# Performance work log

Hardware: AMD Instinct MI355X
Metric: run time of the kernel (lower is better)

The kernel has to match this reference:

```python
import jax, jax.numpy as jnp
import numpy as np

N = 262144       # nodes (4096 graphs * graph_deg 64)
E = 4194304      # edges
D = 64           # node_dim
DEPTH = 3
GRAPH_DEG = 64


def gcn_conv(x, W, b, src, dst, w):
    """PyG GCNConv with self-loops + symmetric norm; masked edges have w=0."""
    h = x @ W                                             # [N, D]
    deg = jax.ops.segment_sum(w, dst, num_segments=N) + 1.0  # +1 self-loop
    dinv = jax.lax.rsqrt(deg)                             # deg >= 1
    norm = dinv[src] * w * dinv[dst]                      # [E]
    agg = jax.ops.segment_sum(h[src] * norm[:, None], dst, num_segments=N)
    agg = agg + h * (dinv * dinv)[:, None]                # self-loop term
    return agg + b


def setup_inputs() -> dict:
    key = jax.random.key(0)
    ks = jax.random.split(key, 24)

    def xavier(k, fan_in, fan_out):
        lim = np.sqrt(6.0 / (fan_in + fan_out))
        return jax.random.uniform(k, (fan_in, fan_out), jnp.float32, -lim, lim)

    inp = {
        "x": jax.random.normal(ks[0], (N, 1), jnp.float32),
        "edge_index": jax.random.randint(ks[1], (2, E), 0, N, jnp.int64),
        "edge_types": jax.random.randint(ks[2], (E,), 0, 5, jnp.int64),
        "node_W": xavier(ks[3], 1, D), "node_b": jnp.zeros((D,), jnp.float32),
        "out1_W": xavier(ks[4], D, D), "out1_b": jnp.zeros((D,), jnp.float32),
        "out2_W": xavier(ks[5], D, 1), "out2_b": jnp.zeros((1,), jnp.float32),
    }
    names = ["W1", "W2", "W3", "W4", "W2b", "W3b", "W4b"]
    for i, n in enumerate(names):
        inp[n] = xavier(ks[6 + i], D, D)
        inp["b" + n[1:]] = jnp.zeros((D,), jnp.float32)
    return inp


def reference(x, edge_index, edge_types,
              node_W, node_b,
              W1, b1, W2, b2, W3, b3, W4, b4,
              W2b, b2b, W3b, b3b, W4b, b4b,
              out1_W, out1_b, out2_W, out2_b):
    src, dst = edge_index[0], edge_index[1]
    w1 = (edge_types == 1).astype(jnp.float32)
    w2 = (edge_types == 2).astype(jnp.float32)
    w3 = (edge_types == 3).astype(jnp.float32)
    w4 = (edge_types == 4).astype(jnp.float32)

    h = x @ node_W + node_b                               # [N, D]
    for _ in range(DEPTH):
        h_new = (gcn_conv(h, W1, b1, src, dst, w1)
                 + gcn_conv(h, W2, b2, src, dst, w2)
                 + gcn_conv(h, W3, b3, src, dst, w3)
                 + gcn_conv(h, W4, b4, src, dst, w4)
                 + gcn_conv(h, W2b, b2b, dst, src, w2)    # reversed edges
                 + gcn_conv(h, W3b, b3b, dst, src, w3)
                 + gcn_conv(h, W4b, b4b, dst, src, w4))
        h = jax.nn.relu(h_new)

    g = h.reshape(-1, GRAPH_DEG, D)                       # [B, deg, D]
    g = jnp.max(g, axis=1)                                # [B, D]
    g = jax.nn.relu(g @ out1_W + out1_b)
    return g @ out2_W + out2_b                            # [B, 1]
```

## Files before the change

kernel.cpp:

```cpp
#include <hip/hip_runtime.h>
#include <stdint.h>

typedef unsigned int u32;
typedef unsigned short u16;
typedef __attribute__((ext_vector_type(8))) short bf16x8;
typedef __attribute__((ext_vector_type(4))) float f32x4;

#define BCAP 16384u

struct Ptr7 { const float* p[7]; };

__device__ __forceinline__ int rfl(int v) { return __builtin_amdgcn_readfirstlane(v); }
__device__ __forceinline__ u16 f2bf(float f) {
    u32 u = __float_as_uint(f);
    u32 r = (u + 0x7FFFu + ((u >> 16) & 1u)) >> 16;
    return (u16)r;
}
__device__ __forceinline__ float bf2f(u16 h) { return __uint_as_float((u32)h << 16); }


__global__ void k_init_cur(u32* __restrict__ g) {
    int i = blockIdx.x * 256 + threadIdx.x;
    if (i < 512) g[i] = (u32)i << 14;
}

__global__ __launch_bounds__(256)
void k_passA(const int* __restrict__ ei, const int* __restrict__ ty, int E,
             u32* __restrict__ gcursor, u32* __restrict__ tmpItems) {
    __shared__ u32 hist[512], gb[512], cur[512];
    int tid = threadIdx.x;
    int e0 = blockIdx.x * 4096;
    int s[16], d[16], t[16];
#pragma unroll
    for (int i = 0; i < 16; i++) {
        int e = e0 + i * 256 + tid;
        if (e < E) { s[i] = ei[e]; d[i] = ei[E + e]; t[i] = ty[e]; }
        else t[i] = 0;
    }
    hist[tid] = 0; hist[tid + 256] = 0;
    __syncthreads();
#pragma unroll
    for (int i = 0; i < 16; i++) {
        if (t[i] >= 1) atomicAdd(&hist[(u32)d[i] >> 9], 1u);
        if (t[i] >= 2) atomicAdd(&hist[(u32)s[i] >> 9], 1u);
    }
    __syncthreads();
    u32 h0 = hist[tid], h1 = hist[tid + 256];
    gb[tid] = h0 ? atomicAdd(&gcursor[tid], h0) : 0u;
    gb[tid + 256] = h1 ? atomicAdd(&gcursor[tid + 256], h1) : 0u;
    cur[tid] = 0; cur[tid + 256] = 0;
    __syncthreads();
#pragma unroll
    for (int i = 0; i < 16; i++) {
        if (t[i] >= 1) {
            u32 b = (u32)d[i] >> 9;
            u32 slot = atomicAdd(&cur[b], 1u);
            u32 pos = gb[b] + slot;
            if (pos < ((b + 1u) << 14))
                tmpItems[pos] = (u32)s[i] | ((u32)(t[i] - 1) << 18) | (((u32)d[i] & 511u) << 21);
        }
        if (t[i] >= 2) {
            u32 b = (u32)s[i] >> 9;
            u32 slot = atomicAdd(&cur[b], 1u);
            u32 pos = gb[b] + slot;
            if (pos < ((b + 1u) << 14))
                tmpItems[pos] = (u32)d[i] | ((u32)(t[i] + 2) << 18) | (((u32)s[i] & 511u) << 21);
        }
    }
}

__global__ __launch_bounds__(256)
void k_passB(const u32* __restrict__ tmpItems, const u32* __restrict__ bucketEnd,
             float* __restrict__ dinv, u16* __restrict__ dinv16,
             u32* __restrict__ kcnt, int N) {
    __shared__ u32 c[512 * 8];
    int b = blockIdx.x, tid = threadIdx.x;
    for (int i = tid; i < 4096; i += 256) c[i] = 0;
    __syncthreads();
    u32 beg = (u32)b << 14;
    u32 end = bucketEnd[b];
    u32 cap = beg + BCAP;
    if (end > cap) end = cap;
    for (u32 i = beg + tid; i < end; i += 256) {
        u32 it = tmpItems[i];
        atomicAdd(&c[(it >> 21) * 8 + ((it >> 18) & 7)], 1u);
    }
    __syncthreads();
    int nodeBase = b << 9;
    for (int i = tid; i < 4096; i += 256) kcnt[(size_t)b * 4096 + i] = c[i];
    for (int l = tid; l < 512; l += 256) {
        int n = nodeBase + l;
#pragma unroll
        for (int k = 0; k < 7; k++) {
            float v = rsqrtf(1.0f + (float)c[l * 8 + k]);
            dinv[k * N + n] = v;
            dinv16[k * N + n] = f2bf(v);
        }
    }
}

__global__ __launch_bounds__(256)
void k_scan1(const u32* __restrict__ kcnt, u32* __restrict__ kofs, u32* __restrict__ bsums) {
    __shared__ u32 lds[256];
    int t = threadIdx.x;
    size_t base = (size_t)blockIdx.x * 8192 + (size_t)t * 32;
    u32 v[32];
    u32 s = 0;
    const uint4* src = (const uint4*)(kcnt + base);
#pragma unroll
    for (int q = 0; q < 8; q++) {
        uint4 c4 = src[q];
        v[q * 4 + 0] = s; s += c4.x;
        v[q * 4 + 1] = s; s += c4.y;
        v[q * 4 + 2] = s; s += c4.z;
        v[q * 4 + 3] = s; s += c4.w;
    }
    lds[t] = s; __syncthreads();
    for (int off = 1; off < 256; off <<= 1) {
        u32 x2 = (t >= off) ? lds[t - off] : 0u;
        __syncthreads();
        lds[t] += x2;
        __syncthreads();
    }
    u32 texcl = lds[t] - s;
    uint4* dst = (uint4*)(kofs + base);
#pragma unroll
    for (int q = 0; q < 8; q++) {
        uint4 o;
        o.x = v[q * 4 + 0] + texcl; o.y = v[q * 4 + 1] + texcl;
        o.z = v[q * 4 + 2] + texcl; o.w = v[q * 4 + 3] + texcl;
        dst[q] = o;
    }
    if (t == 255) bsums[blockIdx.x] = lds[255];
}

__global__ void k_scan2(const u32* __restrict__ bsums, u32* __restrict__ bexcl, int nb) {
    __shared__ u32 lds[256];
    int t = threadIdx.x;
    u32 v = (t < nb) ? bsums[t] : 0u;
    lds[t] = v; __syncthreads();
    for (int off = 1; off < 256; off <<= 1) {
        u32 x2 = (t >= off) ? lds[t - off] : 0u;
        __syncthreads();
        lds[t] += x2;
        __syncthreads();
    }
    if (t < nb) bexcl[t] = lds[t] - v;
}

__global__ __launch_bounds__(256)
void k_scan3(u32* __restrict__ kofs, const u32* __restrict__ bexcl,
             const u32* __restrict__ bsums, u32 M) {
    int t = threadIdx.x;
    size_t base = (size_t)blockIdx.x * 8192 + (size_t)t * 32;
    u32 add = bexcl[blockIdx.x];
    uint4* p4 = (uint4*)(kofs + base);
#pragma unroll
    for (int q = 0; q < 8; q++) {
        uint4 o = p4[q];
        o.x += add; o.y += add; o.z += add; o.w += add;
        p4[q] = o;
    }
    if (blockIdx.x == 255 && t == 255) kofs[M] = add + bsums[255];
}

__global__ __launch_bounds__(256)
void k_passC(const u32* __restrict__ tmpItems, const u32* __restrict__ bucketEnd,
             const u32* __restrict__ kofs, u32* __restrict__ entries) {
    __shared__ u32 cur[4096];
    int b = blockIdx.x, tid = threadIdx.x;
    for (int i = tid; i < 4096; i += 256) cur[i] = kofs[(size_t)b * 4096 + i];
    __syncthreads();
    u32 beg = (u32)b << 14;
    u32 end = bucketEnd[b];
    u32 cap = beg + BCAP;
    if (end > cap) end = cap;
    for (u32 i = beg + tid; i < end; i += 256) {
        u32 it = tmpItems[i];
        u32 k = (it >> 18) & 7u;
        u32 src = it & 0x3FFFFu;
        u32 p = atomicAdd(&cur[(it >> 21) * 8 + k], 1u);
        entries[p] = (k << 28) | (src << 7);
    }
}

__global__ __launch_bounds__(256)
void k_coef_pq(const u32* __restrict__ entries, const u32* __restrict__ kofs,
               const u16* __restrict__ dinv16, const float* __restrict__ dinv,
               const float* __restrict__ x, u16* __restrict__ coef16,
               float* __restrict__ P, float* __restrict__ Q, int N) {
    int i = blockIdx.x * 256 + threadIdx.x;
    u32 beg = kofs[i], end = kofs[i + 1];
    int k = i & 7, n = i >> 3;
    float sP = 0.f, sQ = 0.f;
    for (u32 p = beg; p < end; ++p) {
        u32 src = (entries[p] >> 7) & 0x3FFFFu;
        u16 cb = dinv16[(size_t)k * N + src];
        coef16[p] = cb;
        float cf = bf2f(cb);
        sP += cf * x[src];
        sQ += cf;
    }
    if (k < 7) {
        float dk = dinv[k * N + n];
        float xn = x[n];
        P[i] = dk * (sP + dk * xn);
        Q[i] = dk * (sQ + dk);
    }
}

__global__ void k_bsum(Ptr7 b, float* __restrict__ bsum) {
    int d = threadIdx.x;
    float s = 0.f;
#pragma unroll
    for (int k = 0; k < 7; k++) s += b.p[k][d];
    bsum[d] = s;
}

__global__ void k_uv(const float* __restrict__ nW, const float* __restrict__ nb,
                     Ptr7 W, float* __restrict__ U, float* __restrict__ V) {
    int k = blockIdx.x, d = threadIdx.x;
    const float* Wk = W.p[k];
    float u = 0.f, v = 0.f;
#pragma unroll 8
    for (int j = 0; j < 64; j++) {
        float w = Wk[j * 64 + d];
        u += nW[j] * w;
        v += nb[j] * w;
    }
    U[k * 64 + d] = u;
    V[k * 64 + d] = v;
}

__global__ void k_packW(Ptr7 W, u16* __restrict__ Wp) {
    int k = blockIdx.x;
    int tid = threadIdx.x;
    int ks = tid >> 8, ct = (tid >> 6) & 3, l = tid & 63;
    const float* Wk = W.p[k];
    u16* dst = Wp + (((size_t)(k * 2 + ks) * 4 + ct) * 512 + l * 8);
    int row0 = ks * 32 + (l >> 4) * 8;
    int col = ct * 16 + (l & 15);
#pragma unroll
    for (int i = 0; i < 8; i++) dst[i] = f2bf(Wk[(row0 + i) * 64 + col]);
}

__global__ __launch_bounds__(256)
void k_h1(const float* __restrict__ P, const float* __restrict__ Q,
          const float* __restrict__ U, const float* __restrict__ V,
          const float* __restrict__ bsum, u16* __restrict__ h1) {
    int i = blockIdx.x * 256 + threadIdx.x;
    int n = rfl(i >> 6);
    int d = i & 63;
    float acc = bsum[d];
#pragma unroll
    for (int k = 0; k < 7; k++)
        acc += P[n * 8 + k] * U[k * 64 + d] + Q[n * 8 + k] * V[k * 64 + d];
    h1[((size_t)n << 6) + d] = f2bf(fmaxf(acc, 0.f));
}

#define GACC(PK, CB, HV)                                             \
    {                                                                \
        float cf_ = __uint_as_float((u32)(CB) << 16);                \
        switch ((PK) >> 28) {                                        \
            case 0: a0 = fmaf(cf_, (HV), a0); break;                 \
            case 1: a1 = fmaf(cf_, (HV), a1); break;                 \
            case 2: a2 = fmaf(cf_, (HV), a2); break;                 \
            case 3: a3 = fmaf(cf_, (HV), a3); break;                 \
            case 4: a4 = fmaf(cf_, (HV), a4); break;                 \
            case 5: a5 = fmaf(cf_, (HV), a5); break;                 \
            default: a6 = fmaf(cf_, (HV), a6); break;                \
        }                                                            \
    }
#define HLOAD(PK) bf2f(*(const u16*)(hb + ((PK) & 0x01FFFFFFu)))

__global__ __launch_bounds__(256)
void k_gather(const u16* __restrict__ h, const u32* __restrict__ entries,
              const u16* __restrict__ coef16, const u32* __restrict__ kofs,
              const float* __restrict__ dinv, u16* __restrict__ m, int N, int c0) {
    int lane = threadIdx.x & 63;
    int nl = blockIdx.x * 4 + (threadIdx.x >> 6);
    int n = c0 + nl;
    const char* hb = (const char*)h + 2 * lane;
    u32 beg = (u32)rfl((int)kofs[(size_t)n << 3]);
    u32 end = (u32)rfl((int)kofs[((size_t)n << 3) + 7]);
    float hv = bf2f(h[((size_t)n << 6) + lane]);
    float d0 = dinv[n],         d1 = dinv[N + n],     d2 = dinv[2 * N + n];
    float d3 = dinv[3 * N + n], d4 = dinv[4 * N + n], d5 = dinv[5 * N + n];
    float d6 = dinv[6 * N + n];
    float a0 = d0 * hv, a1 = d1 * hv, a2 = d2 * hv, a3 = d3 * hv;
    float a4 = d4 * hv, a5 = d5 * hv, a6 = d6 * hv;

    u32 base = beg;
    u32 e = 0, cfw = 0;
    if (base + (u32)lane < end) {
        e = __builtin_nontemporal_load(&entries[base + lane]);
        cfw = (u32)__builtin_nontemporal_load(&coef16[base + lane]);
    }
    while (base < end) {
        u32 rem = end - base;
        int cnt = (rem < 64u) ? (int)rem : 64;
        u32 nb2 = base + 64;
        u32 en = 0, cfn = 0;
        if (nb2 + (u32)lane < end) {
            en = __builtin_nontemporal_load(&entries[nb2 + lane]);
            cfn = (u32)__builtin_nontemporal_load(&coef16[nb2 + lane]);
        }
        int j = 0;
        for (; j + 8 <= cnt; j += 8) {
            u32 pk0 = (u32)__builtin_amdgcn_readlane((int)e, j + 0);
            u32 pk1 = (u32)__builtin_amdgcn_readlane((int)e, j + 1);
            u32 pk2 = (u32)__builtin_amdgcn_readlane((int)e, j + 2);
            u32 pk3 = (u32)__builtin_amdgcn_readlane((int)e, j + 3);
            u32 pk4 = (u32)__builtin_amdgcn_readlane((int)e, j + 4);
            u32 pk5 = (u32)__builtin_amdgcn_readlane((int)e, j + 5);
            u32 pk6 = (u32)__builtin_amdgcn_readlane((int)e, j + 6);
            u32 pk7 = (u32)__builtin_amdgcn_readlane((int)e, j + 7);
            u32 cb0 = (u32)__builtin_amdgcn_readlane((int)cfw, j + 0);
            u32 cb1 = (u32)__builtin_amdgcn_readlane((int)cfw, j + 1);
            u32 cb2 = (u32)__builtin_amdgcn_readlane((int)cfw, j + 2);
            u32 cb3 = (u32)__builtin_amdgcn_readlane((int)cfw, j + 3);
            u32 cb4 = (u32)__builtin_amdgcn_readlane((int)cfw, j + 4);
            u32 cb5 = (u32)__builtin_amdgcn_readlane((int)cfw, j + 5);
            u32 cb6 = (u32)__builtin_amdgcn_readlane((int)cfw, j + 6);
            u32 cb7 = (u32)__builtin_amdgcn_readlane((int)cfw, j + 7);
            float h0 = HLOAD(pk0);
            float h1v = HLOAD(pk1);
            float h2v = HLOAD(pk2);
            float h3v = HLOAD(pk3);
            float h4v = HLOAD(pk4);
            float h5v = HLOAD(pk5);
            float h6v = HLOAD(pk6);
            float h7v = HLOAD(pk7);
            GACC(pk0, cb0, h0)
            GACC(pk1, cb1, h1v)
            GACC(pk2, cb2, h2v)
            GACC(pk3, cb3, h3v)
            GACC(pk4, cb4, h4v)
            GACC(pk5, cb5, h5v)
            GACC(pk6, cb6, h6v)
            GACC(pk7, cb7, h7v)
        }
        for (; j + 4 <= cnt; j += 4) {
            u32 pk0 = (u32)__builtin_amdgcn_readlane((int)e, j + 0);
            u32 pk1 = (u32)__builtin_amdgcn_readlane((int)e, j + 1);
            u32 pk2 = (u32)__builtin_amdgcn_readlane((int)e, j + 2);
            u32 pk3 = (u32)__builtin_amdgcn_readlane((int)e, j + 3);
            u32 cb0 = (u32)__builtin_amdgcn_readlane((int)cfw, j + 0);
            u32 cb1 = (u32)__builtin_amdgcn_readlane((int)cfw, j + 1);
            u32 cb2 = (u32)__builtin_amdgcn_readlane((int)cfw, j + 2);
            u32 cb3 = (u32)__builtin_amdgcn_readlane((int)cfw, j + 3);
            float h0 = HLOAD(pk0);
            float h1v = HLOAD(pk1);
            float h2v = HLOAD(pk2);
            float h3v = HLOAD(pk3);
            GACC(pk0, cb0, h0)
            GACC(pk1, cb1, h1v)
            GACC(pk2, cb2, h2v)
            GACC(pk3, cb3, h3v)
        }
        for (; j < cnt; ++j) {
            u32 pk = (u32)__builtin_amdgcn_readlane((int)e, j);
            u32 cb = (u32)__builtin_amdgcn_readlane((int)cfw, j);
            float hval = HLOAD(pk);
            GACC(pk, cb, hval)
        }
        e = en; cfw = cfn; base = nb2;
    }

    u16* mp = m + (size_t)nl * 448 + lane;
    __builtin_nontemporal_store(f2bf(d0 * a0), mp);
    __builtin_nontemporal_store(f2bf(d1 * a1), mp + 64);
    __builtin_nontemporal_store(f2bf(d2 * a2), mp + 128);
    __builtin_nontemporal_store(f2bf(d3 * a3), mp + 192);
    __builtin_nontemporal_store(f2bf(d4 * a4), mp + 256);
    __builtin_nontemporal_store(f2bf(d5 * a5), mp + 320);
    __builtin_nontemporal_store(f2bf(d6 * a6), mp + 384);
}

__global__ __launch_bounds__(256)
void k_gemm(const u16* __restrict__ m, const u16* __restrict__ Wp,
            const float* __restrict__ bsum, u16* __restrict__ hout, int c0) {
    int tid = threadIdx.x;
    int w = tid >> 6, l = tid & 63;
    int nb = blockIdx.x << 6;
    const u16* arow = m + (size_t)(nb + (w << 4) + (l & 15)) * 448 + ((l >> 4) << 3);
    const u16* bp = Wp + (size_t)l * 8;
    f32x4 acc0 = {0,0,0,0}, acc1 = {0,0,0,0}, acc2 = {0,0,0,0}, acc3 = {0,0,0,0};
#pragma unroll
    for (int kk = 0; kk < 14; kk++) {
        bf16x8 a  = __builtin_nontemporal_load((const bf16x8*)(arow + kk * 32));
        bf16x8 b0 = *(const bf16x8*)(bp + (size_t)(kk * 4 + 0) * 512);
        bf16x8 b1 = *(const bf16x8*)(bp + (size_t)(kk * 4 + 1) * 512);
        bf16x8 b2 = *(const bf16x8*)(bp + (size_t)(kk * 4 + 2) * 512);
        bf16x8 b3 = *(const bf16x8*)(bp + (size_t)(kk * 4 + 3) * 512);
        acc0 = __builtin_amdgcn_mfma_f32_16x16x32_bf16(a, b0, acc0, 0, 0, 0);
        acc1 = __builtin_amdgcn_mfma_f32_16x16x32_bf16(a, b1, acc1, 0, 0, 0);
        acc2 = __builtin_amdgcn_mfma_f32_16x16x32_bf16(a, b2, acc2, 0, 0, 0);
        acc3 = __builtin_amdgcn_mfma_f32_16x16x32_bf16(a, b3, acc3, 0, 0, 0);
    }
    int rl = (l >> 4) << 2, cl = l & 15;
    int rowg = c0 + nb + (w << 4) + rl;
    f32x4 accs[4] = {acc0, acc1, acc2, acc3};
#pragma unroll
    for (int ct = 0; ct < 4; ct++) {
        int col = ct * 16 + cl;
        float bv = bsum[col];
#pragma unroll
        for (int reg = 0; reg < 4; reg++) {
            float vv = fmaxf(accs[ct][reg] + bv, 0.f);
            hout[(size_t)(rowg + reg) * 64 + col] = f2bf(vv);
        }
    }
}

__global__ __launch_bounds__(256)
void k_head(const u16* __restrict__ h, const float* __restrict__ w1,
            const float* __restrict__ b1, const float* __restrict__ w2,
            const float* __restrict__ b2, float* __restrict__ out) {
    __shared__ float gmax[4][64];
    __shared__ float gl[64];
    __shared__ float t1p[4][64];
    int b = blockIdx.x;
    int tid = threadIdx.x;
    int d = tid & 63, rg = tid >> 6;
    const u16* hb = h + (size_t)b * 64 * 64;
    float pm = -1e30f;
#pragma unroll
    for (int i = 0; i < 16; i++) pm = fmaxf(pm, bf2f(hb[(rg * 16 + i) * 64 + d]));
    gmax[rg][d] = pm; __syncthreads();
    if (rg == 0) gl[d] = fmaxf(fmaxf(gmax[0][d], gmax[1][d]), fmaxf(gmax[2][d], gmax[3][d]));
    __syncthreads();
    float s = 0.f;
#pragma unroll
    for (int i = 0; i < 16; i++) { int dd = rg * 16 + i; s += gl[dd] * w1[dd * 64 + d]; }
    t1p[rg][d] = s; __syncthreads();
    if (rg == 0) {
        float t1 = fmaxf(t1p[0][d] + t1p[1][d] + t1p[2][d] + t1p[3][d] + b1[d], 0.f);
        float v = t1 * w2[d];
        for (int off = 32; off; off >>= 1) v += __shfl_down(v, off, 64);
        if (d == 0) out[b] = v + b2[0];
    }
}

extern "C" void kernel_launch(void* const* d_in, const int* in_sizes, int n_in,
                              void* d_out, int out_size, void* d_ws, size_t ws_size,
                              hipStream_t stream) {
    const float* x     = (const float*)d_in[0];
    const int*   ei    = (const int*)d_in[1];
    const int*   ty    = (const int*)d_in[2];
    const float* nodeW = (const float*)d_in[3];
    const float* nodeb = (const float*)d_in[4];
    const float* out1W = (const float*)d_in[5];
    const float* out1b = (const float*)d_in[6];
    const float* out2W = (const float*)d_in[7];
    const float* out2b = (const float*)d_in[8];

    Ptr7 W, B;
    W.p[0] = (const float*)d_in[9];  B.p[0] = (const float*)d_in[10];
    W.p[1] = (const float*)d_in[11]; B.p[1] = (const float*)d_in[12];
    W.p[2] = (const float*)d_in[13]; B.p[2] = (const float*)d_in[14];
    W.p[3] = (const float*)d_in[15]; B.p[3] = (const float*)d_in[16];
    W.p[4] = (const float*)d_in[17]; B.p[4] = (const float*)d_in[18];
    W.p[5] = (const float*)d_in[19]; B.p[5] = (const float*)d_in[20];
    W.p[6] = (const float*)d_in[21]; B.p[6] = (const float*)d_in[22];

    const int N = in_sizes[0];
    const int E = in_sizes[2];

    char* p = (char*)d_ws;
    auto carve = [&](size_t bytes) { void* r = (void*)p; p += (bytes + 255) & ~(size_t)255; return r; };
    u16*   hA       = (u16*)carve((size_t)N * 64 * 2);
    u16*   hB       = (u16*)carve((size_t)N * 64 * 2);
    u32*   entries  = (u32*)carve((size_t)2 * E * 4 + 256);
    u16*   coef16   = (u16*)carve((size_t)2 * E * 2 + 128);
    float* dinv     = (float*)carve((size_t)7 * N * 4);
    u16*   dinv16   = (u16*)carve((size_t)7 * N * 2);
    u32*   kcnt     = (u32*)carve((size_t)8 * N * 4);
    u32*   kofs     = (u32*)carve(((size_t)8 * N + 1) * 4);
    float* P        = (float*)carve((size_t)N * 8 * 4);
    float* Q        = (float*)carve((size_t)N * 8 * 4);
    float* U        = (float*)carve(7 * 64 * 4);
    float* V        = (float*)carve(7 * 64 * 4);
    float* bsum     = (float*)carve(256);
    u16*   Wp       = (u16*)carve((size_t)7 * 2 * 4 * 512 * 2);
    u32*   gcursor  = (u32*)carve(512 * 4);
    u32*   bsums    = (u32*)carve(1024);
    u32*   bexcl    = (u32*)carve(1024);
    size_t used = (size_t)(p - (char*)d_ws);
    size_t avail = (ws_size > used) ? (ws_size - used) : 0;
    u32*   tmpItems = (u32*)p;
    u16*   m        = (u16*)p;
    size_t chunkNodes = (avail / (448 * 2)) & ~(size_t)63;
    if (chunkNodes < 64) chunkNodes = 64;
    if (chunkNodes > 131072) chunkNodes = 131072;
    if (chunkNodes > (size_t)N) chunkNodes = (size_t)N;
    (void)n_in; (void)out_size;

    k_init_cur<<<2, 256, 0, stream>>>(gcursor);
    k_passA<<<(E + 4095) / 4096, 256, 0, stream>>>(ei, ty, E, gcursor, tmpItems);
    k_passB<<<512, 256, 0, stream>>>(tmpItems, gcursor, dinv, dinv16, kcnt, N);
    k_scan1<<<256, 256, 0, stream>>>(kcnt, kofs, bsums);
    k_scan2<<<1, 256, 0, stream>>>(bsums, bexcl, 256);
    k_scan3<<<256, 256, 0, stream>>>(kofs, bexcl, bsums, (u32)8 * N);
    k_passC<<<512, 256, 0, stream>>>(tmpItems, gcursor, kofs, entries);
    k_coef_pq<<<(8 * N) / 256, 256, 0, stream>>>(entries, kofs, dinv16, dinv, x,
                                                 coef16, P, Q, N);

    k_bsum<<<1, 64, 0, stream>>>(B, bsum);
    k_uv<<<7, 64, 0, stream>>>(nodeW, nodeb, W, U, V);
    k_packW<<<7, 512, 0, stream>>>(W, Wp);

    k_h1<<<(N * 64) / 256, 256, 0, stream>>>(P, Q, U, V, bsum, hA);

    u16* hcur = hA;
    u16* hnext = hB;
    for (int depth = 0; depth < 2; depth++) {
        for (int c0 = 0; c0 < N; c0 += (int)chunkNodes) {
            int cn = (int)(((size_t)(N - c0) < chunkNodes) ? (size_t)(N - c0) : chunkNodes);
            k_gather<<<cn / 4, 256, 0, stream>>>(hcur, entries, coef16, kofs, dinv, m, N, c0);
            k_gemm<<<cn / 64, 256, 0, stream>>>(m, Wp, bsum, hnext, c0);
        }
        u16* t = hcur; hcur = hnext; hnext = t;
    }

    k_head<<<N / 64, 256, 0, stream>>>(hcur, out1W, out1b, out2W, out2b, (float*)d_out);
}
```

Measured before the change: 943.5 us.

## Pad per-node edge lists to multiples of eight and use scalar loads in gather

The degree pass now writes a padding count into the eighth key slot so each node's edge segment is padded to a multiple of eight entries, and coef/PQ skips that slot. The gather kernel replaces its vector-load-plus-readlane broadcast of edge entries and coefficients with inline s_load_dwordx8/x4 scalar loads of eight entries at a time, then accumulates per edge type. This aims to cut VALU readlane overhead and vector memory traffic for edge metadata. The trade-off is a full lgkmcnt wait on every eight-edge chunk, which serialises scalar latency and removes the previous double-buffered prefetch, and correctness depends on the padding keeping scalar loads aligned.

```diff
diff --git a/kernel.cpp b/kernel.cpp
--- a/kernel.cpp
+++ b/kernel.cpp
@@ -5,6 +5,8 @@
 typedef unsigned short u16;
 typedef __attribute__((ext_vector_type(8))) short bf16x8;
 typedef __attribute__((ext_vector_type(4))) float f32x4;
+typedef __attribute__((ext_vector_type(8))) unsigned int u32x8_t;
+typedef __attribute__((ext_vector_type(4))) unsigned int u32x4_t;
 
 #define BCAP 16384u
 
@@ -87,15 +89,19 @@
     }
     __syncthreads();
     int nodeBase = b << 9;
-    for (int i = tid; i < 4096; i += 256) kcnt[(size_t)b * 4096 + i] = c[i];
     for (int l = tid; l < 512; l += 256) {
         int n = nodeBase + l;
+        u32 tot = 0;
 #pragma unroll
         for (int k = 0; k < 7; k++) {
-            float v = rsqrtf(1.0f + (float)c[l * 8 + k]);
+            u32 g = c[l * 8 + k];
+            tot += g;
+            kcnt[(size_t)b * 4096 + l * 8 + k] = g;
+            float v = rsqrtf(1.0f + (float)g);
             dinv[k * N + n] = v;
             dinv16[k * N + n] = f2bf(v);
         }
+        kcnt[(size_t)b * 4096 + l * 8 + 7] = (8u - (tot & 7u)) & 7u;
     }
 }
 
@@ -190,8 +196,9 @@
                const float* __restrict__ x, u16* __restrict__ coef16,
                float* __restrict__ P, float* __restrict__ Q, int N) {
     int i = blockIdx.x * 256 + threadIdx.x;
+    int k = i & 7, n = i >> 3;
+    if (k == 7) return;
     u32 beg = kofs[i], end = kofs[i + 1];
-    int k = i & 7, n = i >> 3;
     float sP = 0.f, sQ = 0.f;
     for (u32 p = beg; p < end; ++p) {
         u32 src = (entries[p] >> 7) & 0x3FFFFu;
@@ -201,12 +208,10 @@
         sP += cf * x[src];
         sQ += cf;
     }
-    if (k < 7) {
-        float dk = dinv[k * N + n];
-        float xn = x[n];
-        P[i] = dk * (sP + dk * xn);
-        Q[i] = dk * (sQ + dk);
-    }
+    float dk = dinv[k * N + n];
+    float xn = x[n];
+    P[i] = dk * (sP + dk * xn);
+    Q[i] = dk * (sQ + dk);
 }
 
 __global__ void k_bsum(Ptr7 b, float* __restrict__ bsum) {
@@ -258,21 +263,6 @@
     h1[((size_t)n << 6) + d] = f2bf(fmaxf(acc, 0.f));
 }
 
-#define GACC(PK, CB, HV)                                             \
-    {                                                                \
-        float cf_ = __uint_as_float((u32)(CB) << 16);                \
-        switch ((PK) >> 28) {                                        \
-            case 0: a0 = fmaf(cf_, (HV), a0); break;                 \
-            case 1: a1 = fmaf(cf_, (HV), a1); break;                 \
-            case 2: a2 = fmaf(cf_, (HV), a2); break;                 \
-            case 3: a3 = fmaf(cf_, (HV), a3); break;                 \
-            case 4: a4 = fmaf(cf_, (HV), a4); break;                 \
-            case 5: a5 = fmaf(cf_, (HV), a5); break;                 \
-            default: a6 = fmaf(cf_, (HV), a6); break;                \
-        }                                                            \
-    }
-#define HLOAD(PK) bf2f(*(const u16*)(hb + ((PK) & 0x01FFFFFFu)))
-
 __global__ __launch_bounds__(256)
 void k_gather(const u16* __restrict__ h, const u32* __restrict__ entries,
               const u16* __restrict__ coef16, const u32* __restrict__ kofs,
@@ -280,7 +270,6 @@
     int lane = threadIdx.x & 63;
     int nl = blockIdx.x * 4 + (threadIdx.x >> 6);
     int n = c0 + nl;
-    const char* hb = (const char*)h + 2 * lane;
     u32 beg = (u32)rfl((int)kofs[(size_t)n << 3]);
     u32 end = (u32)rfl((int)kofs[((size_t)n << 3) + 7]);
     float hv = bf2f(h[((size_t)n << 6) + lane]);
@@ -290,81 +279,39 @@
     float a0 = d0 * hv, a1 = d1 * hv, a2 = d2 * hv, a3 = d3 * hv;
     float a4 = d4 * hv, a5 = d5 * hv, a6 = d6 * hv;
 
-    u32 base = beg;
-    u32 e = 0, cfw = 0;
-    if (base + (u32)lane < end) {
-        e = __builtin_nontemporal_load(&entries[base + lane]);
-        cfw = (u32)__builtin_nontemporal_load(&coef16[base + lane]);
-    }
-    while (base < end) {
-        u32 rem = end - base;
-        int cnt = (rem < 64u) ? (int)rem : 64;
-        u32 nb2 = base + 64;
-        u32 en = 0, cfn = 0;
-        if (nb2 + (u32)lane < end) {
-            en = __builtin_nontemporal_load(&entries[nb2 + lane]);
-            cfn = (u32)__builtin_nontemporal_load(&coef16[nb2 + lane]);
-        }
-        int j = 0;
-        for (; j + 8 <= cnt; j += 8) {
-            u32 pk0 = (u32)__builtin_amdgcn_readlane((int)e, j + 0);
-            u32 pk1 = (u32)__builtin_amdgcn_readlane((int)e, j + 1);
-            u32 pk2 = (u32)__builtin_amdgcn_readlane((int)e, j + 2);
-            u32 pk3 = (u32)__builtin_amdgcn_readlane((int)e, j + 3);
-            u32 pk4 = (u32)__builtin_amdgcn_readlane((int)e, j + 4);
-            u32 pk5 = (u32)__builtin_amdgcn_readlane((int)e, j + 5);
-            u32 pk6 = (u32)__builtin_amdgcn_readlane((int)e, j + 6);
-            u32 pk7 = (u32)__builtin_amdgcn_readlane((int)e, j + 7);
-            u32 cb0 = (u32)__builtin_amdgcn_readlane((int)cfw, j + 0);
-            u32 cb1 = (u32)__builtin_amdgcn_readlane((int)cfw, j + 1);
-            u32 cb2 = (u32)__builtin_amdgcn_readlane((int)cfw, j + 2);
-            u32 cb3 = (u32)__builtin_amdgcn_readlane((int)cfw, j + 3);
-            u32 cb4 = (u32)__builtin_amdgcn_readlane((int)cfw, j + 4);
-            u32 cb5 = (u32)__builtin_amdgcn_readlane((int)cfw, j + 5);
-            u32 cb6 = (u32)__builtin_amdgcn_readlane((int)cfw, j + 6);
-            u32 cb7 = (u32)__builtin_amdgcn_readlane((int)cfw, j + 7);
-            float h0 = HLOAD(pk0);
-            float h1v = HLOAD(pk1);
-            float h2v = HLOAD(pk2);
-            float h3v = HLOAD(pk3);
-            float h4v = HLOAD(pk4);
-            float h5v = HLOAD(pk5);
-            float h6v = HLOAD(pk6);
-            float h7v = HLOAD(pk7);
-            GACC(pk0, cb0, h0)
-            GACC(pk1, cb1, h1v)
-            GACC(pk2, cb2, h2v)
-            GACC(pk3, cb3, h3v)
-            GACC(pk4, cb4, h4v)
-            GACC(pk5, cb5, h5v)
-            GACC(pk6, cb6, h6v)
-            GACC(pk7, cb7, h7v)
-        }
-        for (; j + 4 <= cnt; j += 4) {
-            u32 pk0 = (u32)__builtin_amdgcn_readlane((int)e, j + 0);
-            u32 pk1 = (u32)__builtin_amdgcn_readlane((int)e, j + 1);
-            u32 pk2 = (u32)__builtin_amdgcn_readlane((int)e, j + 2);
-            u32 pk3 = (u32)__builtin_amdgcn_readlane((int)e, j + 3);
-            u32 cb0 = (u32)__builtin_amdgcn_readlane((int)cfw, j + 0);
-            u32 cb1 = (u32)__builtin_amdgcn_readlane((int)cfw, j + 1);
-            u32 cb2 = (u32)__builtin_amdgcn_readlane((int)cfw, j + 2);
-            u32 cb3 = (u32)__builtin_amdgcn_readlane((int)cfw, j + 3);
-            float h0 = HLOAD(pk0);
-            float h1v = HLOAD(pk1);
-            float h2v = HLOAD(pk2);
-            float h3v = HLOAD(pk3);
-            GACC(pk0, cb0, h0)
-            GACC(pk1, cb1, h1v)
-            GACC(pk2, cb2, h2v)
-            GACC(pk3, cb3, h3v)
-        }
-        for (; j < cnt; ++j) {
-            u32 pk = (u32)__builtin_amdgcn_readlane((int)e, j);
-            u32 cb = (u32)__builtin_amdgcn_readlane((int)cfw, j);
-            float hval = HLOAD(pk);
-            GACC(pk, cb, hval)
-        }
-        e = en; cfw = cfn; base = nb2;
+    const u32* ep = entries + beg;
+    const u32* cp = (const u32*)(coef16 + beg);
+    for (u32 base = beg; base < end; base += 8) {
+        u32x8_t ev;
+        u32x4_t cv;
+        asm("s_load_dwordx8 %0, %2, 0x0\n\t"
+            "s_load_dwordx4 %1, %3, 0x0\n\t"
+            "s_waitcnt lgkmcnt(0)"
+            : "=s"(ev), "=s"(cv)
+            : "s"(ep), "s"(cp));
+        ep += 8; cp += 4;
+        int cnt = (int)(end - base);
+        if (cnt > 8) cnt = 8;
+#pragma unroll
+        for (int j = 0; j < 8; j++) {
+            if (j < cnt) {
+                u32 pk = ev[j];
+                u32 cw = cv[j >> 1];
+                u32 cb = (j & 1) ? (cw >> 16) : (cw & 0xFFFFu);
+                float cf = __uint_as_float(cb << 16);
+                u32 off = (pk & 0x0FFFFFFFu) >> 1;
+                float hval = bf2f(h[off + (u32)lane]);
+                switch (pk >> 28) {
+                    case 0: a0 = fmaf(cf, hval, a0); break;
+                    case 1: a1 = fmaf(cf, hval, a1); break;
+                    case 2: a2 = fmaf(cf, hval, a2); break;
+                    case 3: a3 = fmaf(cf, hval, a3); break;
+                    case 4: a4 = fmaf(cf, hval, a4); break;
+                    case 5: a5 = fmaf(cf, hval, a5); break;
+                    default: a6 = fmaf(cf, hval, a6); break;
+                }
+            }
+        }
     }
 
     u16* mp = m + (size_t)nl * 448 + lane;
```

Result: slower. 1.259 ms (+33.4%).

## Fuse gather and MFMA GEMM into one kernel with LDS-staged messages

Applied to the files above, without the earlier changes.

Merges the per-node neighbor gather and the 448x64 bf16 MFMA projection into a single kernel. Each 512-thread block gathers 32 nodes into LDS and then runs the GEMM from LDS, so the intermediate message buffer is no longer written to and re-read from global memory and the chunked launch loop goes away. It also makes threads for the unused eighth edge-type slot return early in the coef kernel. The cost is a large LDS footprint and a block barrier between the gather and GEMM phases, and the GEMM step now has far fewer MFMAs per wave, which may limit occupancy or overlap.

```diff
diff --git a/kernel.cpp b/kernel.cpp
--- a/kernel.cpp
+++ b/kernel.cpp
@@ -190,8 +190,9 @@
                const float* __restrict__ x, u16* __restrict__ coef16,
                float* __restrict__ P, float* __restrict__ Q, int N) {
     int i = blockIdx.x * 256 + threadIdx.x;
+    int k = i & 7, n = i >> 3;
+    if (k == 7) return;
     u32 beg = kofs[i], end = kofs[i + 1];
-    int k = i & 7, n = i >> 3;
     float sP = 0.f, sQ = 0.f;
     for (u32 p = beg; p < end; ++p) {
         u32 src = (entries[p] >> 7) & 0x3FFFFu;
@@ -201,12 +202,10 @@
         sP += cf * x[src];
         sQ += cf;
     }
-    if (k < 7) {
-        float dk = dinv[k * N + n];
-        float xn = x[n];
-        P[i] = dk * (sP + dk * xn);
-        Q[i] = dk * (sQ + dk);
-    }
+    float dk = dinv[k * N + n];
+    float xn = x[n];
+    P[i] = dk * (sP + dk * xn);
+    Q[i] = dk * (sQ + dk);
 }
 
 __global__ void k_bsum(Ptr7 b, float* __restrict__ bsum) {
@@ -271,145 +270,113 @@
             default: a6 = fmaf(cf_, (HV), a6); break;                \
         }                                                            \
     }
-#define HLOAD(PK) bf2f(*(const u16*)(hb + ((PK) & 0x01FFFFFFu)))
-
-__global__ __launch_bounds__(256)
-void k_gather(const u16* __restrict__ h, const u32* __restrict__ entries,
-              const u16* __restrict__ coef16, const u32* __restrict__ kofs,
-              const float* __restrict__ dinv, u16* __restrict__ m, int N, int c0) {
-    int lane = threadIdx.x & 63;
-    int nl = blockIdx.x * 4 + (threadIdx.x >> 6);
-    int n = c0 + nl;
-    const char* hb = (const char*)h + 2 * lane;
-    u32 beg = (u32)rfl((int)kofs[(size_t)n << 3]);
-    u32 end = (u32)rfl((int)kofs[((size_t)n << 3) + 7]);
-    float hv = bf2f(h[((size_t)n << 6) + lane]);
-    float d0 = dinv[n],         d1 = dinv[N + n],     d2 = dinv[2 * N + n];
-    float d3 = dinv[3 * N + n], d4 = dinv[4 * N + n], d5 = dinv[5 * N + n];
-    float d6 = dinv[6 * N + n];
-    float a0 = d0 * hv, a1 = d1 * hv, a2 = d2 * hv, a3 = d3 * hv;
-    float a4 = d4 * hv, a5 = d5 * hv, a6 = d6 * hv;
-
-    u32 base = beg;
-    u32 e = 0, cfw = 0;
-    if (base + (u32)lane < end) {
-        e = __builtin_nontemporal_load(&entries[base + lane]);
-        cfw = (u32)__builtin_nontemporal_load(&coef16[base + lane]);
-    }
-    while (base < end) {
-        u32 rem = end - base;
-        int cnt = (rem < 64u) ? (int)rem : 64;
-        u32 nb2 = base + 64;
-        u32 en = 0, cfn = 0;
-        if (nb2 + (u32)lane < end) {
-            en = __builtin_nontemporal_load(&entries[nb2 + lane]);
-            cfn = (u32)__builtin_nontemporal_load(&coef16[nb2 + lane]);
+#define HLOAD(PK) bf2f(h[(((PK) & 0x0FFFFFFFu) >> 1) + (u32)lane])
+
+__global__ __launch_bounds__(512, 8)
+void k_fused(const u16* __restrict__ h, const u32* __restrict__ entries,
+             const u16* __restrict__ coef16, const u32* __restrict__ kofs,
+             const float* __restrict__ dinv, const u16* __restrict__ Wp,
+             const float* __restrict__ bsum, u16* __restrict__ hout, int N) {
+    __shared__ u16 mlds[32 * 456];
+    int tid = threadIdx.x;
+    int w = tid >> 6, lane = tid & 63;
+    int nb = blockIdx.x << 5;
+
+    for (int rr = 0; rr < 4; ++rr) {
+        int nn = (w << 2) + rr;
+        int n = nb + nn;
+        u32 beg = (u32)rfl((int)kofs[(size_t)n << 3]);
+        u32 end = (u32)rfl((int)kofs[((size_t)n << 3) + 7]);
+        float hv = bf2f(h[((size_t)n << 6) + lane]);
+        float d0 = dinv[n],         d1 = dinv[N + n],     d2 = dinv[2 * N + n];
+        float d3 = dinv[3 * N + n], d4 = dinv[4 * N + n], d5 = dinv[5 * N + n];
+        float d6 = dinv[6 * N + n];
+        float a0 = d0 * hv, a1 = d1 * hv, a2 = d2 * hv, a3 = d3 * hv;
+        float a4 = d4 * hv, a5 = d5 * hv, a6 = d6 * hv;
+
+        u32 base = beg;
+        u32 e = 0, cfw = 0;
+        if (base + (u32)lane < end) {
+            e = __builtin_nontemporal_load(&entries[base + lane]);
+            cfw = (u32)__builtin_nontemporal_load(&coef16[base + lane]);
         }
-        int j = 0;
-        for (; j + 8 <= cnt; j += 8) {
-            u32 pk0 = (u32)__builtin_amdgcn_readlane((int)e, j + 0);
-            u32 pk1 = (u32)__builtin_amdgcn_readlane((int)e, j + 1);
-            u32 pk2 = (u32)__builtin_amdgcn_readlane((int)e, j + 2);
-            u32 pk3 = (u32)__builtin_amdgcn_readlane((int)e, j + 3);
-            u32 pk4 = (u32)__builtin_amdgcn_readlane((int)e, j + 4);
-            u32 pk5 = (u32)__builtin_amdgcn_readlane((int)e, j + 5);
-            u32 pk6 = (u32)__builtin_amdgcn_readlane((int)e, j + 6);
-            u32 pk7 = (u32)__builtin_amdgcn_readlane((int)e, j + 7);
-            u32 cb0 = (u32)__builtin_amdgcn_readlane((int)cfw, j + 0);
-            u32 cb1 = (u32)__builtin_amdgcn_readlane((int)cfw, j + 1);
-            u32 cb2 = (u32)__builtin_amdgcn_readlane((int)cfw, j + 2);
-            u32 cb3 = (u32)__builtin_amdgcn_readlane((int)cfw, j + 3);
-            u32 cb4 = (u32)__builtin_amdgcn_readlane((int)cfw, j + 4);
-            u32 cb5 = (u32)__builtin_amdgcn_readlane((int)cfw, j + 5);
-            u32 cb6 = (u32)__builtin_amdgcn_readlane((int)cfw, j + 6);
-            u32 cb7 = (u32)__builtin_amdgcn_readlane((int)cfw, j + 7);
-            float h0 = HLOAD(pk0);
-            float h1v = HLOAD(pk1);
-            float h2v = HLOAD(pk2);
-            float h3v = HLOAD(pk3);
-            float h4v = HLOAD(pk4);
-            float h5v = HLOAD(pk5);
-            float h6v = HLOAD(pk6);
-            float h7v = HLOAD(pk7);
-            GACC(pk0, cb0, h0)
-            GACC(pk1, cb1, h1v)
-            GACC(pk2, cb2, h2v)
-            GACC(pk3, cb3, h3v)
-            GACC(pk4, cb4, h4v)
-            GACC(pk5, cb5, h5v)
-            GACC(pk6, cb6, h6v)
-            GACC(pk7, cb7, h7v)
+        while (base < end) {
+            u32 rem = end - base;
+            int cnt = (rem < 64u) ? (int)rem : 64;
+            u32 nb2 = base + 64;
+            u32 en = 0, cfn = 0;
+            if (nb2 + (u32)lane < end) {
+                en = __builtin_nontemporal_load(&entries[nb2 + lane]);
+                cfn = (u32)__builtin_nontemporal_load(&coef16[nb2 + lane]);
+            }
+            int j = 0;
+            for (; j + 8 <= cnt; j += 8) {
+                u32 pk0 = (u32)__builtin_amdgcn_readlane((int)e, j + 0);
+                u32 pk1 = (u32)__builtin_amdgcn_readlane((int)e, j + 1);
+                u32 pk2 = (u32)__builtin_amdgcn_readlane((int)e, j + 2);
+                u32 pk3 = (u32)__builtin_amdgcn_readlane((int)e, j + 3);
+                u32 pk4 = (u32)__builtin_amdgcn_readlane((int)e, j + 4);
+                u32 pk5 = (u32)__builtin_amdgcn_readlane((int)e, j + 5);
+                u32 pk6 = (u32)__builtin_amdgcn_readlane((int)e, j + 6);
+                u32 pk7 = (u32)__builtin_amdgcn_readlane((int)e, j + 7);
+                u32 cb0 = (u32)__builtin_amdgcn_readlane((int)cfw, j + 0);
+                u32 cb1 = (u32)__builtin_amdgcn_readlane((int)cfw, j + 1);
+                u32 cb2 = (u32)__builtin_amdgcn_readlane((int)cfw, j + 2);
+                u32 cb3 = (u32)__builtin_amdgcn_readlane((int)cfw, j + 3);
+                u32 cb4 = (u32)__builtin_amdgcn_readlane((int)cfw, j + 4);
+                u32 cb5 = (u32)__builtin_amdgcn_readlane((int)cfw, j + 5);
+                u32 cb6 = (u32)__builtin_amdgcn_readlane((int)cfw, j + 6);
+                u32 cb7 = (u32)__builtin_amdgcn_readlane((int)cfw, j + 7);
+                float h0 = HLOAD(pk0);
+                float h1v = HLOAD(pk1);
+                float h2v = HLOAD(pk2);
+                float h3v = HLOAD(pk3);
+                float h4v = HLOAD(pk4);
+                float h5v = HLOAD(pk5);
+                float h6v = HLOAD(pk6);
+                float h7v = HLOAD(pk7);
+                GACC(pk0, cb0, h0)
+                GACC(pk1, cb1, h1v)
+                GACC(pk2, cb2, h2v)
+                GACC(pk3, cb3, h3v)
+                GACC(pk4, cb4, h4v)
+                GACC(pk5, cb5, h5v)
+                GACC(pk6, cb6, h6v)
+                GACC(pk7, cb7, h7v)
+            }
+            for (; j < cnt; ++j) {
+                u32 pk = (u32)__builtin_amdgcn_readlane((int)e, j);
+                u32 cb = (u32)__builtin_amdgcn_readlane((int)cfw, j);
+                float hval = HLOAD(pk);
+                GACC(pk, cb, hval)
+            }
+            e = en; cfw = cfn; base = nb2;
         }
-        for (; j + 4 <= cnt; j += 4) {
-            u32 pk0 = (u32)__builtin_amdgcn_readlane((int)e, j + 0);
-            u32 pk1 = (u32)__builtin_amdgcn_readlane((int)e, j + 1);
-            u32 pk2 = (u32)__builtin_amdgcn_readlane((int)e, j + 2);
-            u32 pk3 = (u32)__builtin_amdgcn_readlane((int)e, j + 3);
-            u32 cb0 = (u32)__builtin_amdgcn_readlane((int)cfw, j + 0);
-            u32 cb1 = (u32)__builtin_amdgcn_readlane((int)cfw, j + 1);
-            u32 cb2 = (u32)__builtin_amdgcn_readlane((int)cfw, j + 2);
-            u32 cb3 = (u32)__builtin_amdgcn_readlane((int)cfw, j + 3);
-            float h0 = HLOAD(pk0);
-            float h1v = HLOAD(pk1);
-            float h2v = HLOAD(pk2);
-            float h3v = HLOAD(pk3);
-            GACC(pk0, cb0, h0)
-            GACC(pk1, cb1, h1v)
-            GACC(pk2, cb2, h2v)
-            GACC(pk3, cb3, h3v)
-        }
-        for (; j < cnt; ++j) {
-            u32 pk = (u32)__builtin_amdgcn_readlane((int)e, j);
-            u32 cb = (u32)__builtin_amdgcn_readlane((int)cfw, j);
-            float hval = HLOAD(pk);
-            GACC(pk, cb, hval)
-        }
-        e = en; cfw = cfn; base = nb2;
-    }
-
-    u16* mp = m + (size_t)nl * 448 + lane;
-    __builtin_nontemporal_store(f2bf(d0 * a0), mp);
-    __builtin_nontemporal_store(f2bf(d1 * a1), mp + 64);
-    __builtin_nontemporal_store(f2bf(d2 * a2), mp + 128);
-    __builtin_nontemporal_store(f2bf(d3 * a3), mp + 192);
-    __builtin_nontemporal_store(f2bf(d4 * a4), mp + 256);
-    __builtin_nontemporal_store(f2bf(d5 * a5), mp + 320);
-    __builtin_nontemporal_store(f2bf(d6 * a6), mp + 384);
-}
-
-__global__ __launch_bounds__(256)
-void k_gemm(const u16* __restrict__ m, const u16* __restrict__ Wp,
-            const float* __restrict__ bsum, u16* __restrict__ hout, int c0) {
-    int tid = threadIdx.x;
-    int w = tid >> 6, l = tid & 63;
-    int nb = blockIdx.x << 6;
-    const u16* arow = m + (size_t)(nb + (w << 4) + (l & 15)) * 448 + ((l >> 4) << 3);
-    const u16* bp = Wp + (size_t)l * 8;
-    f32x4 acc0 = {0,0,0,0}, acc1 = {0,0,0,0}, acc2 = {0,0,0,0}, acc3 = {0,0,0,0};
+
+        u16* mp = mlds + nn * 456 + lane;
+        mp[0]   = f2bf(d0 * a0); mp[64]  = f2bf(d1 * a1); mp[128] = f2bf(d2 * a2);
+        mp[192] = f2bf(d3 * a3); mp[256] = f2bf(d4 * a4); mp[320] = f2bf(d5 * a5);
+        mp[384] = f2bf(d6 * a6);
+    }
+    __syncthreads();
+
+    int rg = w >> 2, cq = w & 3;
+    const u16* bp = Wp + (size_t)cq * 512 + (size_t)lane * 8;
+    const u16* arow = mlds + (rg * 16 + (lane & 15)) * 456 + ((lane >> 4) << 3);
+    f32x4 acc = {0, 0, 0, 0};
 #pragma unroll
     for (int kk = 0; kk < 14; kk++) {
-        bf16x8 a  = __builtin_nontemporal_load((const bf16x8*)(arow + kk * 32));
-        bf16x8 b0 = *(const bf16x8*)(bp + (size_t)(kk * 4 + 0) * 512);
-        bf16x8 b1 = *(const bf16x8*)(bp + (size_t)(kk * 4 + 1) * 512);
-        bf16x8 b2 = *(const bf16x8*)(bp + (size_t)(kk * 4 + 2) * 512);
-        bf16x8 b3 = *(const bf16x8*)(bp + (size_t)(kk * 4 + 3) * 512);
-        acc0 = __builtin_amdgcn_mfma_f32_16x16x32_bf16(a, b0, acc0, 0, 0, 0);
-        acc1 = __builtin_amdgcn_mfma_f32_16x16x32_bf16(a, b1, acc1, 0, 0, 0);
-        acc2 = __builtin_amdgcn_mfma_f32_16x16x32_bf16(a, b2, acc2, 0, 0, 0);
-        acc3 = __builtin_amdgcn_mfma_f32_16x16x32_bf16(a, b3, acc3, 0, 0, 0);
-    }
-    int rl = (l >> 4) << 2, cl = l & 15;
-    int rowg = c0 + nb + (w << 4) + rl;
-    f32x4 accs[4] = {acc0, acc1, acc2, acc3};
-#pragma unroll
-    for (int ct = 0; ct < 4; ct++) {
-        int col = ct * 16 + cl;
-        float bv = bsum[col];
-#pragma unroll
-        for (int reg = 0; reg < 4; reg++) {
-            float vv = fmaxf(accs[ct][reg] + bv, 0.f);
-            hout[(size_t)(rowg + reg) * 64 + col] = f2bf(vv);
-        }
+        bf16x8 a = *(const bf16x8*)(arow + kk * 32);
+        bf16x8 b = *(const bf16x8*)(bp + (size_t)kk * 4 * 512);
+        acc = __builtin_amdgcn_mfma_f32_16x16x32_bf16(a, b, acc, 0, 0, 0);
+    }
+    int col = cq * 16 + (lane & 15);
+    int row0 = nb + rg * 16 + ((lane >> 4) << 2);
+    float bv = bsum[col];
+#pragma unroll
+    for (int reg = 0; reg < 4; reg++) {
+        float vv = fmaxf(acc[reg] + bv, 0.f);
+        hout[(size_t)(row0 + reg) * 64 + col] = f2bf(vv);
     }
 }
 
@@ -486,15 +453,8 @@
     u32*   gcursor  = (u32*)carve(512 * 4);
     u32*   bsums    = (u32*)carve(1024);
     u32*   bexcl    = (u32*)carve(1024);
-    size_t used = (size_t)(p - (char*)d_ws);
-    size_t avail = (ws_size > used) ? (ws_size - used) : 0;
     u32*   tmpItems = (u32*)p;
-    u16*   m        = (u16*)p;
-    size_t chunkNodes = (avail / (448 * 2)) & ~(size_t)63;
-    if (chunkNodes < 64) chunkNodes = 64;
-    if (chunkNodes > 131072) chunkNodes = 131072;
-    if (chunkNodes > (size_t)N) chunkNodes = (size_t)N;
-    (void)n_in; (void)out_size;
+    (void)n_in; (void)out_size; (void)ws_size;
 
     k_init_cur<<<2, 256, 0, stream>>>(gcursor);
     k_passA<<<(E + 4095) / 4096, 256, 0, stream>>>(ei, ty, E, gcursor, tmpItems);
@@ -512,16 +472,8 @@
 
     k_h1<<<(N * 64) / 256, 256, 0, stream>>>(P, Q, U, V, bsum, hA);
 
-    u16* hcur = hA;
-    u16* hnext = hB;
-    for (int depth = 0; depth < 2; depth++) {
-        for (int c0 = 0; c0 < N; c0 += (int)chunkNodes) {
-            int cn = (int)(((size_t)(N - c0) < chunkNodes) ? (size_t)(N - c0) : chunkNodes);
-            k_gather<<<cn / 4, 256, 0, stream>>>(hcur, entries, coef16, kofs, dinv, m, N, c0);
-            k_gemm<<<cn / 64, 256, 0, stream>>>(m, Wp, bsum, hnext, c0);
-        }
-        u16* t = hcur; hcur = hnext; hnext = t;
-    }
-
-    k_head<<<N / 64, 256, 0, stream>>>(hcur, out1W, out1b, out2W, out2b, (float*)d_out);
-}
+    k_fused<<<N / 32, 512, 0, stream>>>(hA, entries, coef16, kofs, dinv, Wp, bsum, hB, N);
+    k_fused<<<N / 32, 512, 0, stream>>>(hB, entries, coef16, kofs, dinv, Wp, bsum, hA, N);
+
+    k_head<<<N / 64, 256, 0, stream>>>(hA, out1W, out1b, out2W, out2b, (float*)d_out);
+}
```

New measurement: 787.1 us. -16.6%, faster.
